# Performance work log

Hardware: AMD Instinct MI355X
Metric: run time of the kernel (lower is better)

The kernel has to match this reference:

```python
import jax, jax.numpy as jnp
import numpy as np

N_HEADS = 12
N_GROUPS = 32
EPS = 1e-5


def setup_inputs() -> dict:
    key = jax.random.key(0)
    ks = jax.random.split(key, 6)
    B, C, H, W = 8, 768, 32, 32
    EC, S = 768, 256
    x = jax.random.normal(ks[0], (B, C, H, W), dtype=jnp.float32)
    encoder_out = jax.random.normal(ks[1], (B, EC, S), dtype=jnp.float32)
    gn_w = jnp.ones((C,), jnp.float32)
    gn_b = jnp.zeros((C,), jnp.float32)
    qkv_w = jax.random.normal(ks[2], (3 * C, C), dtype=jnp.float32) * 0.02
    qkv_b = jnp.zeros((3 * C,), jnp.float32)
    enc_w = jax.random.normal(ks[3], (2 * C, EC), dtype=jnp.float32) * 0.02
    enc_b = jnp.zeros((2 * C,), jnp.float32)
    proj_w = jax.random.normal(ks[4], (C, C), dtype=jnp.float32) * 0.02
    proj_b = jnp.zeros((C,), jnp.float32)
    return {"x": x, "encoder_out": encoder_out, "gn_w": gn_w, "gn_b": gn_b,
            "qkv_w": qkv_w, "qkv_b": qkv_b, "enc_w": enc_w, "enc_b": enc_b,
            "proj_w": proj_w, "proj_b": proj_b}


def _group_norm(x, w, b):
    # x: [B, C, T]
    B, C, T = x.shape
    xg = x.reshape(B, N_GROUPS, C // N_GROUPS, T)
    mean = jnp.mean(xg, axis=(2, 3), keepdims=True)
    var = jnp.var(xg, axis=(2, 3), keepdims=True)
    xn = ((xg - mean) * jax.lax.rsqrt(var + EPS)).reshape(B, C, T)
    return xn * w[None, :, None] + b[None, :, None]


def reference(x, encoder_out, gn_w, gn_b, qkv_w, qkv_b, enc_w, enc_b, proj_w, proj_b):
    B, C, Hs, Ws = x.shape
    T = Hs * Ws
    ch = C // N_HEADS
    xf = x.reshape(B, C, T)
    xn = _group_norm(xf, gn_w, gn_b)
    # 1x1 conv == channel matmul
    qkv = jnp.einsum('oc,bct->bot', qkv_w, xn) + qkv_b[None, :, None]  # [B, 3C, T]
    # torch layout: per-head contiguous blocks of [q, k, v]
    qkv = qkv.reshape(B * N_HEADS, 3 * ch, T)
    q, k, v = qkv[:, :ch], qkv[:, ch:2 * ch], qkv[:, 2 * ch:]
    ekv = jnp.einsum('oc,bcs->bos', enc_w, encoder_out) + enc_b[None, :, None]  # [B, 2C, S]
    ekv = ekv.reshape(B * N_HEADS, 2 * ch, -1)
    ek, ev = ekv[:, :ch], ekv[:, ch:]
    k = jnp.concatenate([ek, k], axis=-1)  # [BH, ch, S+T]
    v = jnp.concatenate([ev, v], axis=-1)
    scale = 1.0 / np.sqrt(np.sqrt(ch))
    w = jnp.einsum('bct,bcs->bts', q * scale, k * scale)  # [BH, T, S+T]
    w = jax.nn.softmax(w.astype(jnp.float32), axis=-1).astype(q.dtype)
    a = jnp.einsum('bts,bcs->bct', w, v).reshape(B, C, T)
    h = jnp.einsum('oc,bct->bot', proj_w, a) + proj_b[None, :, None]
    return (xf + h).reshape(B, C, Hs, Ws)
```

## Files before the change

### kernel.cpp

```cpp
#include <hip/hip_runtime.h>

typedef __attribute__((ext_vector_type(8))) short bf16x8;
typedef __attribute__((ext_vector_type(4))) float f32x4;
typedef __attribute__((ext_vector_type(16))) float f32x16;
typedef __attribute__((ext_vector_type(4))) float float4v;
typedef __attribute__((ext_vector_type(4))) unsigned short ushort4v;
typedef __attribute__((ext_vector_type(8))) unsigned short ushort8v;

#define DEVINL __device__ __forceinline__


DEVINL unsigned short f2bf(float f) {
  union { float f; unsigned u; } v; v.f = f;
  unsigned r = (v.u + 0x7fffu + ((v.u >> 16) & 1u)) >> 16;
  return (unsigned short)r;
}
DEVINL float bf2f(unsigned short h) {
  union { unsigned u; float f; } v; v.u = ((unsigned)h) << 16;
  return v.f;
}
DEVINL float exp2a(float x) {
  float r; asm("v_exp_f32 %0, %1" : "=v"(r) : "v"(x)); return r;
}
DEVINL unsigned cvtpk(float lo, float hi) {
  unsigned r;
  asm("v_cvt_pk_bf16_f32 %0, %1, %2" : "=v"(r) : "v"(lo), "v"(hi));
  return r;
}
DEVINL void gload16(const void* g, void* l) {
  __builtin_amdgcn_global_load_lds(
      (const __attribute__((address_space(1))) unsigned*)g,
      (__attribute__((address_space(3))) unsigned*)l, 16, 0, 0);
}
DEVINL void plswap(unsigned& a, unsigned& b) {
  asm("v_permlane32_swap_b32 %0, %1" : "+v"(a), "+v"(b));
}
DEVINL bf16x8 mkfrag(unsigned a, unsigned b, unsigned c, unsigned d) {
  union { unsigned u[4]; bf16x8 v; } x;
  x.u[0] = a; x.u[1] = b; x.u[2] = c; x.u[3] = d;
  return x.v;
}
#define WAITV0 asm volatile("s_waitcnt vmcnt(0)" ::: "memory")
#define RBAR  __builtin_amdgcn_s_barrier()

__global__ __launch_bounds__(256) void k_cvt3(const float* __restrict__ s0,
                                              const float* __restrict__ s1,
                                              const float* __restrict__ s2,
                                              unsigned short* __restrict__ d) {
  int i = blockIdx.x * 256 + threadIdx.x;
  const float* s; int off;
  if (i < 442368)      { s = s0; off = i; }
  else if (i < 737280) { s = s1; off = i - 442368; }
  else                 { s = s2; off = i - 737280; }
  float4v v = *(const float4v*)(s + (size_t)off * 4);
  ushort4v o;
  o[0] = f2bf(v[0]); o[1] = f2bf(v[1]); o[2] = f2bf(v[2]); o[3] = f2bf(v[3]);
  *(ushort4v*)(d + (size_t)i * 4) = o;
}

__global__ __launch_bounds__(256) void k_gn(const float* __restrict__ x,
                                            const float* __restrict__ gw,
                                            const float* __restrict__ gb,
                                            unsigned short* __restrict__ xnt) {
  int g = blockIdx.x, b = blockIdx.y, tid = threadIdx.x;
  const float* xb = x + ((size_t)b * 768 + g * 24) * 1024;
  float s = 0.f, ss = 0.f;
  for (int i = tid; i < 6144; i += 256) {
    float4v v = *(const float4v*)(xb + (size_t)i * 4);
    s += v[0] + v[1] + v[2] + v[3];
    ss += v[0] * v[0] + v[1] * v[1] + v[2] * v[2] + v[3] * v[3];
  }
  #pragma unroll
  for (int o = 32; o > 0; o >>= 1) { s += __shfl_down(s, o); ss += __shfl_down(ss, o); }
  __shared__ float rs[4], rss[4], stat[2];
  int w = tid >> 6;
  if ((tid & 63) == 0) { rs[w] = s; rss[w] = ss; }
  __syncthreads();
  if (tid == 0) {
    float S = rs[0] + rs[1] + rs[2] + rs[3], SS = rss[0] + rss[1] + rss[2] + rss[3];
    float mean = S / 24576.f;
    float var = SS / 24576.f - mean * mean;
    stat[0] = mean; stat[1] = rsqrtf(fmaxf(var, 0.f) + 1e-5f);
  }
  __syncthreads();
  float mean = stat[0], rstd = stat[1];
  float wv[24], bv[24];
  #pragma unroll
  for (int c = 0; c < 24; ++c) { wv[c] = gw[g * 24 + c]; bv[c] = gb[g * 24 + c]; }
  for (int it = 0; it < 4; ++it) {
    int t = it * 256 + tid;
    ushort8v ov[3];
    #pragma unroll
    for (int c = 0; c < 24; ++c) {
      float v = xb[(size_t)c * 1024 + t];
      ov[c >> 3][c & 7] = f2bf((v - mean) * rstd * wv[c] + bv[c]);
    }
    ushort8v* dst = (ushort8v*)(xnt + ((size_t)(b * 1024 + t)) * 768 + g * 24);
    dst[0] = ov[0]; dst[1] = ov[1]; dst[2] = ov[2];
  }
}

__global__ __launch_bounds__(256) void k_enc_tr(const float* __restrict__ enc,
                                                unsigned short* __restrict__ et) {
  int ct = blockIdx.x * 64, st = blockIdx.y * 64, b = blockIdx.z, tid = threadIdx.x;
  __shared__ unsigned short L[64 * 72];
  #pragma unroll
  for (int it = 0; it < 4; ++it) {
    int idx = it * 256 + tid; int r = idx >> 4, ch = idx & 15;
    float4v v = *(const float4v*)(enc + ((size_t)(b * 768 + ct + r)) * 256 + st + ch * 4);
    ushort4v o;
    o[0] = f2bf(v[0]); o[1] = f2bf(v[1]); o[2] = f2bf(v[2]); o[3] = f2bf(v[3]);
    *(ushort4v*)&L[r * 72 + ch * 4] = o;
  }
  __syncthreads();
  #pragma unroll
  for (int it = 0; it < 2; ++it) {
    int idx = it * 256 + tid; int s = idx >> 3, ch = idx & 7;
    ushort8v o;
    #pragma unroll
    for (int j = 0; j < 8; ++j) o[j] = L[(ch * 8 + j) * 72 + s];
    *(ushort8v*)(et + ((size_t)(b * 256 + st + s)) * 768 + ct + ch * 8) = o;
  }
}

__global__ __launch_bounds__(256) void k_vcat(const unsigned short* __restrict__ qkvt,
                                              const unsigned short* __restrict__ ekvt,
                                              unsigned short* __restrict__ vcat) {
  int s0 = blockIdx.x * 64, bh = blockIdx.y, b = bh / 12, h = bh % 12, tid = threadIdx.x;
  __shared__ unsigned short L[64 * 72];
  #pragma unroll
  for (int it = 0; it < 2; ++it) {
    int idx = it * 256 + tid; int s = idx >> 3, ch = idx & 7;
    int sg = s0 + s;
    const unsigned short* src = (sg < 256)
        ? ekvt + ((size_t)(b * 256 + sg)) * 1536 + h * 128 + 64 + ch * 8
        : qkvt + ((size_t)(b * 1024 + sg - 256)) * 2304 + h * 192 + 128 + ch * 8;
    *(ushort8v*)&L[s * 72 + ch * 8] = *(const ushort8v*)src;
  }
  __syncthreads();
  #pragma unroll
  for (int it = 0; it < 2; ++it) {
    int idx = it * 256 + tid; int c = idx >> 3, ch = idx & 7;
    ushort8v o;
    #pragma unroll
    for (int j = 0; j < 8; ++j) o[j] = L[(ch * 8 + j) * 72 + c];
    *(ushort8v*)(vcat + ((size_t)bh * 64 + c) * 1280 + s0 + ch * 8) = o;
  }
}

template <int EPI, int BM>
__global__ __launch_bounds__(256, 4) void k_gemm(const unsigned short* __restrict__ A,
                                                 const unsigned short* __restrict__ B,
                                                 const float* __restrict__ bias,
                                                 const float* __restrict__ resid,
                                                 void* __restrict__ outp,
                                                 int N, int K,
                                                 long sA, long sB, long sO, long sR) {
  constexpr int MI = BM / 32;
  int bz = blockIdx.z;
  int m0 = blockIdx.x * BM, n0 = blockIdx.y * 128;
  const unsigned short* Ab = A + (size_t)bz * sA + (size_t)m0 * K;
  const unsigned short* Bb = B + (size_t)bz * sB + (size_t)n0 * K;
  __shared__ unsigned short As[2][BM * 32], Bs[2][128 * 32];
  int tid = threadIdx.x, lane = tid & 63, w = tid >> 6;
  int ln = lane & 15, lg = lane >> 4;
  int wm = (w >> 1) * (BM / 2), wn = (w & 1) * 64;
  int sr = tid >> 2, sc = tid & 3;
  const unsigned short* gA = Ab + (size_t)sr * K + ((sc ^ (sr & 3)) * 8);
  const unsigned short* gB = Bb + (size_t)sr * K + ((sc ^ (sr & 3)) * 8);
  int swz = (lg ^ (ln & 3)) * 8;

  f32x4 acc[MI][4];
  #pragma unroll
  for (int i = 0; i < MI; ++i)
    #pragma unroll
    for (int j = 0; j < 4; ++j) acc[i][j] = (f32x4){0.f, 0.f, 0.f, 0.f};

  auto stageAB = [&](int buf, int k0) {
    unsigned short* ad = &As[buf][0] + w * 512;
    unsigned short* bd = &Bs[buf][0] + w * 512;
    gload16(gA + k0, ad);
    if constexpr (BM == 128) gload16(gA + (size_t)64 * K + k0, ad + 2048);
    gload16(gB + k0, bd);
    gload16(gB + (size_t)64 * K + k0, bd + 2048);
  };
  auto WAITP = [&] {
    if constexpr (BM == 128) asm volatile("s_waitcnt vmcnt(4)" ::: "memory");
    else                     asm volatile("s_waitcnt vmcnt(3)" ::: "memory");
  };
  auto comp = [&](int buf) {
    bf16x8 af[MI], bfv[4];
    #pragma unroll
    for (int i = 0; i < MI; ++i) af[i] = *(const bf16x8*)&As[buf][(wm + i * 16 + ln) * 32 + swz];
    #pragma unroll
    for (int j = 0; j < 4; ++j) bfv[j] = *(const bf16x8*)&Bs[buf][(wn + j * 16 + ln) * 32 + swz];
    #pragma unroll
    for (int i = 0; i < MI; ++i)
      #pragma unroll
      for (int j = 0; j < 4; ++j)
        acc[i][j] = __builtin_amdgcn_mfma_f32_16x16x32_bf16(af[i], bfv[j], acc[i][j], 0, 0, 0);
  };

  int nk = K >> 5;
  stageAB(0, 0);
  stageAB(1, 32);
  WAITP();
  RBAR;
  int cur = 0;
  for (int kt = 0; kt < nk; ++kt) {
    comp(cur);
    if (kt + 2 < nk) {
      RBAR;
      stageAB(cur, (kt + 2) * 32);
      WAITP();
      RBAR;
    } else if (kt + 1 < nk) {
      WAITV0;
      RBAR;
    }
    cur ^= 1;
  }

  #pragma unroll
  for (int i = 0; i < MI; ++i) {
    #pragma unroll
    for (int j = 0; j < 4; ++j) {
      #pragma unroll
      for (int r = 0; r < 4; ++r) {
        int row = m0 + wm + i * 16 + lg * 4 + r;
        int col = n0 + wn + j * 16 + ln;
        float v = acc[i][j][r];
        if (EPI == 0) {
          v += bias[col];
          ((unsigned short*)outp)[(size_t)bz * sO + (size_t)row * N + col] = f2bf(v);
        } else {
          v += bias[row] + resid[(size_t)bz * sR + (size_t)row * N + col];
          ((float*)outp)[(size_t)bz * sO + (size_t)row * N + col] = v;
        }
      }
    }
  }
}

__global__ __launch_bounds__(256, 3) void k_attn(const unsigned short* __restrict__ qkvt,
                                                 const unsigned short* __restrict__ ekvt,
                                                 const unsigned short* __restrict__ vcat,
                                                 unsigned short* __restrict__ at) {
  int bid = blockIdx.x;
  int swb = (bid & 7) * 96 + (bid >> 3);
  int t0 = (swb & 7) * 128, bh = swb >> 3, b = bh / 12, h = bh % 12;
  int tid = threadIdx.x, w = tid >> 6, lane = tid & 63;
  int ql = lane & 31, hi = lane >> 5;
  __shared__ unsigned short Ks[2][4096], Vs[2][4096];

  const float QSC = 0.125f * 1.44269504089f;
  bf16x8 aq[4];
  const unsigned short* qrow = qkvt + ((size_t)(b * 1024 + t0 + w * 32 + ql)) * 2304 + h * 192;
  #pragma unroll
  for (int jc = 0; jc < 4; ++jc) {
    ushort8v qv = *(const ushort8v*)(qrow + jc * 16 + hi * 8);
    bf16x8 o;
    #pragma unroll
    for (int e = 0; e < 8; ++e) o[e] = (short)f2bf(bf2f(qv[e]) * QSC);
    aq[jc] = o;
  }

  int rloc = w * 16 + (lane >> 3);
  int chunk = (lane & 7) ^ (lane >> 3);
  const unsigned short* ke_st = ekvt + ((size_t)(b * 256 + rloc)) * 1536 + h * 128 + chunk * 8;
  const unsigned short* kq_st = qkvt + ((long)b * 1024 - 256 + rloc) * 2304 + h * 192 + 64 + chunk * 8;
  const unsigned short* v_st  = vcat + ((size_t)(bh * 64 + rloc)) * 1280 + chunk * 8;
  unsigned short* kd = &Ks[0][0] + w * 1024;
  unsigned short* vd = &Vs[0][0] + w * 1024;

  auto stage = [&](int nb, int tn) {
    const unsigned short* ks;
    size_t rstep;
    if (tn < 4) { ks = ke_st + (size_t)tn * 64 * 1536; rstep = 8 * 1536; }
    else        { ks = kq_st + (size_t)tn * 64 * 2304; rstep = 8 * 2304; }
    unsigned short* kdd = kd + nb * 4096;
    unsigned short* vdd = vd + nb * 4096;
    const unsigned short* vs = v_st + tn * 64;
    gload16(ks, kdd);
    gload16(ks + rstep, kdd + 512);
    gload16(vs, vdd);
    gload16(vs + 8 * 1280, vdd + 512);
  };

  stage(0, 0);
  WAITV0;
  __syncthreads();

  f32x16 acc0, acc1;
  #pragma unroll
  for (int r = 0; r < 16; ++r) { acc0[r] = 0.f; acc1[r] = 0.f; }
  float l = 0.f;
  int xp = (ql & 7) << 4;

  for (int t = 0; t < 20; ++t) {
    int cur = t & 1;
    if (t < 19) stage(cur ^ 1, t + 1);

    f32x16 sA0, sB0, sA1, sB1;
    #pragma unroll
    for (int r = 0; r < 16; ++r) { sA0[r] = 0.f; sB0[r] = 0.f; sA1[r] = 0.f; sB1[r] = 0.f; }
    const char* kbase = (const char*)&Ks[cur][0] + ql * 128;
    __builtin_amdgcn_s_setprio(1);
    #pragma unroll
    for (int jc = 0; jc < 4; ++jc) {
      int off = (jc * 32 + hi * 16) ^ xp;
      bf16x8 k0f = *(const bf16x8*)(kbase + off);
      bf16x8 k1f = *(const bf16x8*)(kbase + 4096 + off);
      if (jc & 1) {
        sB0 = __builtin_amdgcn_mfma_f32_32x32x16_bf16(k0f, aq[jc], sB0, 0, 0, 0);
        sB1 = __builtin_amdgcn_mfma_f32_32x32x16_bf16(k1f, aq[jc], sB1, 0, 0, 0);
      } else {
        sA0 = __builtin_amdgcn_mfma_f32_32x32x16_bf16(k0f, aq[jc], sA0, 0, 0, 0);
        sA1 = __builtin_amdgcn_mfma_f32_32x32x16_bf16(k1f, aq[jc], sA1, 0, 0, 0);
      }
    }
    __builtin_amdgcn_s_setprio(0);
    f32x16 sf0 = sA0 + sB0;
    f32x16 sf1 = sA1 + sB1;

    float pe[32];
    #pragma unroll
    for (int i = 0; i < 16; ++i) pe[i] = exp2a(sf0[i]);
    #pragma unroll
    for (int i = 0; i < 16; ++i) pe[16 + i] = exp2a(sf1[i]);

    const char* vbase = (const char*)&Vs[cur][0] + ql * 128;
    #pragma unroll
    for (int sb = 0; sb < 2; ++sb) {
      unsigned pk[8];
      #pragma unroll
      for (int i = 0; i < 8; ++i)
        pk[i] = cvtpk(pe[sb * 16 + 2 * i], pe[sb * 16 + 2 * i + 1]);
      plswap(pk[0], pk[2]);
      plswap(pk[1], pk[3]);
      plswap(pk[4], pk[6]);
      plswap(pk[5], pk[7]);
      bf16x8 fj0 = mkfrag(pk[0], pk[1], pk[2], pk[3]);
      bf16x8 fj1 = mkfrag(pk[4], pk[5], pk[6], pk[7]);
      __builtin_amdgcn_s_setprio(1);
      #pragma unroll
      for (int jj = 0; jj < 2; ++jj) {
        int off = (sb * 64 + jj * 32 + hi * 16) ^ xp;
        bf16x8 v0f = *(const bf16x8*)(vbase + off);
        bf16x8 v1f = *(const bf16x8*)(vbase + 4096 + off);
        bf16x8 pf = jj ? fj1 : fj0;
        acc0 = __builtin_amdgcn_mfma_f32_32x32x16_bf16(v0f, pf, acc0, 0, 0, 0);
        acc1 = __builtin_amdgcn_mfma_f32_32x32x16_bf16(v1f, pf, acc1, 0, 0, 0);
      }
      __builtin_amdgcn_s_setprio(0);
    }

    float s0 = 0.f, s1 = 0.f, s2 = 0.f, s3 = 0.f;
    #pragma unroll
    for (int i = 0; i < 8; ++i) {
      s0 += pe[i]; s1 += pe[8 + i]; s2 += pe[16 + i]; s3 += pe[24 + i];
    }
    l += (s0 + s1) + (s2 + s3);

    if (t < 19) WAITV0;
    __syncthreads();
  }

  l += __shfl_xor(l, 32);
  float rl = 1.f / l;
  unsigned short* orow = at + ((size_t)(b * 1024 + t0 + w * 32 + ql)) * 768 + h * 64;
  #pragma unroll
  for (int cb = 0; cb < 2; ++cb) {
    #pragma unroll
    for (int g = 0; g < 4; ++g) {
      int c = cb * 32 + g * 8 + hi * 4;
      ushort4v o;
      #pragma unroll
      for (int i = 0; i < 4; ++i) {
        float v = (cb ? acc1[g * 4 + i] : acc0[g * 4 + i]) * rl;
        o[i] = f2bf(v);
      }
      *(ushort4v*)(orow + c) = o;
    }
  }
}

extern "C" void kernel_launch(void* const* d_in, const int* in_sizes, int n_in,
                              void* d_out, int out_size, void* d_ws, size_t ws_size,
                              hipStream_t stream) {
  const float* x      = (const float*)d_in[0];
  const float* enc    = (const float*)d_in[1];
  const float* gn_w   = (const float*)d_in[2];
  const float* gn_b   = (const float*)d_in[3];
  const float* qkv_w  = (const float*)d_in[4];
  const float* qkv_b  = (const float*)d_in[5];
  const float* enc_w  = (const float*)d_in[6];
  const float* enc_b  = (const float*)d_in[7];
  const float* proj_w = (const float*)d_in[8];
  const float* proj_b = (const float*)d_in[9];
  float* out = (float*)d_out;

  char* ws = (char*)d_ws;
  unsigned short* w_qkv = (unsigned short*)(ws + 0);
  unsigned short* w_enc = (unsigned short*)(ws + 3538944);
  unsigned short* w_prj = (unsigned short*)(ws + 5898240);
  unsigned short* xn_t  = (unsigned short*)(ws + 7077888);
  unsigned short* enc_t = (unsigned short*)(ws + 19660800);
  unsigned short* qkv_t = (unsigned short*)(ws + 22806528);
  unsigned short* ekv_t = (unsigned short*)(ws + 60555264);
  unsigned short* vcat  = (unsigned short*)(ws + 66846720);
  unsigned short* a_t   = xn_t;

  k_cvt3<<<3456, 256, 0, stream>>>(qkv_w, enc_w, proj_w, w_qkv);
  k_gn<<<dim3(32, 8), 256, 0, stream>>>(x, gn_w, gn_b, xn_t);
  k_enc_tr<<<dim3(12, 4, 8), 256, 0, stream>>>(enc, enc_t);
  k_gemm<0, 128><<<dim3(64, 18, 1), 256, 0, stream>>>(xn_t, w_qkv, qkv_b, nullptr, qkv_t,
                                                      2304, 768, 0L, 0L, 0L, 0L);
  k_gemm<0, 64><<<dim3(32, 12, 1), 256, 0, stream>>>(enc_t, w_enc, enc_b, nullptr, ekv_t,
                                                     1536, 768, 0L, 0L, 0L, 0L);
  k_vcat<<<dim3(20, 96), 256, 0, stream>>>(qkv_t, ekv_t, vcat);
  k_attn<<<dim3(768), 256, 0, stream>>>(qkv_t, ekv_t, vcat, a_t);
  k_gemm<1, 64><<<dim3(12, 8, 8), 256, 0, stream>>>(w_prj, a_t, proj_b, x, out,
                                                    1024, 768, 0L, 786432L, 786432L, 786432L);
}
```

Before: 174.3 us.

## Software-pipeline attention: triple-buffer K/V and overlap next QK with current PV

Moves the attention loop to a three-stage LDS ring buffer. It prefetches two tiles ahead and computes the next tile's QK scores before the current tile's exp/PV work, so MFMA and exp/pack work from different tiles can interleave. The exp-sum is folded into the pack loop and the split A/B accumulators for QK are dropped. This costs more LDS (which may reduce occupancy at 3 blocks/CU), more live registers for the carried score tiles, and a serial MFMA dependency chain in QK.

```diff
diff --git a/kernel.cpp b/kernel.cpp
--- a/kernel.cpp
+++ b/kernel.cpp
@@ -41,6 +41,7 @@
   return x.v;
 }
 #define WAITV0 asm volatile("s_waitcnt vmcnt(0)" ::: "memory")
+#define WAITV4 asm volatile("s_waitcnt vmcnt(4)" ::: "memory")
 #define RBAR  __builtin_amdgcn_s_barrier()
 
 __global__ __launch_bounds__(256) void k_cvt3(const float* __restrict__ s0,
@@ -251,7 +252,7 @@
   int t0 = (swb & 7) * 128, bh = swb >> 3, b = bh / 12, h = bh % 12;
   int tid = threadIdx.x, w = tid >> 6, lane = tid & 63;
   int ql = lane & 31, hi = lane >> 5;
-  __shared__ unsigned short Ks[2][4096], Vs[2][4096];
+  __shared__ unsigned short Ks[3][4096], Vs[3][4096];
 
   const float QSC = 0.125f * 1.44269504089f;
   bf16x8 aq[4];
@@ -270,16 +271,14 @@
   const unsigned short* ke_st = ekvt + ((size_t)(b * 256 + rloc)) * 1536 + h * 128 + chunk * 8;
   const unsigned short* kq_st = qkvt + ((long)b * 1024 - 256 + rloc) * 2304 + h * 192 + 64 + chunk * 8;
   const unsigned short* v_st  = vcat + ((size_t)(bh * 64 + rloc)) * 1280 + chunk * 8;
-  unsigned short* kd = &Ks[0][0] + w * 1024;
-  unsigned short* vd = &Vs[0][0] + w * 1024;
 
   auto stage = [&](int nb, int tn) {
     const unsigned short* ks;
     size_t rstep;
     if (tn < 4) { ks = ke_st + (size_t)tn * 64 * 1536; rstep = 8 * 1536; }
     else        { ks = kq_st + (size_t)tn * 64 * 2304; rstep = 8 * 2304; }
-    unsigned short* kdd = kd + nb * 4096;
-    unsigned short* vdd = vd + nb * 4096;
+    unsigned short* kdd = &Ks[nb][0] + w * 1024;
+    unsigned short* vdd = &Vs[nb][0] + w * 1024;
     const unsigned short* vs = v_st + tn * 64;
     gload16(ks, kdd);
     gload16(ks + rstep, kdd + 512);
@@ -287,55 +286,54 @@
     gload16(vs + 8 * 1280, vdd + 512);
   };
 
-  stage(0, 0);
-  WAITV0;
-  __syncthreads();
-
-  f32x16 acc0, acc1;
-  #pragma unroll
-  for (int r = 0; r < 16; ++r) { acc0[r] = 0.f; acc1[r] = 0.f; }
-  float l = 0.f;
   int xp = (ql & 7) << 4;
-
-  for (int t = 0; t < 20; ++t) {
-    int cur = t & 1;
-    if (t < 19) stage(cur ^ 1, t + 1);
-
-    f32x16 sA0, sB0, sA1, sB1;
-    #pragma unroll
-    for (int r = 0; r < 16; ++r) { sA0[r] = 0.f; sB0[r] = 0.f; sA1[r] = 0.f; sB1[r] = 0.f; }
-    const char* kbase = (const char*)&Ks[cur][0] + ql * 128;
+  auto qk = [&](int nb, f32x16& s0v, f32x16& s1v) {
+    const char* kbase = (const char*)&Ks[nb][0] + ql * 128;
     __builtin_amdgcn_s_setprio(1);
     #pragma unroll
     for (int jc = 0; jc < 4; ++jc) {
       int off = (jc * 32 + hi * 16) ^ xp;
       bf16x8 k0f = *(const bf16x8*)(kbase + off);
       bf16x8 k1f = *(const bf16x8*)(kbase + 4096 + off);
-      if (jc & 1) {
-        sB0 = __builtin_amdgcn_mfma_f32_32x32x16_bf16(k0f, aq[jc], sB0, 0, 0, 0);
-        sB1 = __builtin_amdgcn_mfma_f32_32x32x16_bf16(k1f, aq[jc], sB1, 0, 0, 0);
-      } else {
-        sA0 = __builtin_amdgcn_mfma_f32_32x32x16_bf16(k0f, aq[jc], sA0, 0, 0, 0);
-        sA1 = __builtin_amdgcn_mfma_f32_32x32x16_bf16(k1f, aq[jc], sA1, 0, 0, 0);
-      }
+      s0v = __builtin_amdgcn_mfma_f32_32x32x16_bf16(k0f, aq[jc], s0v, 0, 0, 0);
+      s1v = __builtin_amdgcn_mfma_f32_32x32x16_bf16(k1f, aq[jc], s1v, 0, 0, 0);
     }
     __builtin_amdgcn_s_setprio(0);
-    f32x16 sf0 = sA0 + sB0;
-    f32x16 sf1 = sA1 + sB1;
-
-    float pe[32];
-    #pragma unroll
-    for (int i = 0; i < 16; ++i) pe[i] = exp2a(sf0[i]);
-    #pragma unroll
-    for (int i = 0; i < 16; ++i) pe[16 + i] = exp2a(sf1[i]);
-
-    const char* vbase = (const char*)&Vs[cur][0] + ql * 128;
+  };
+
+  f32x16 acc0, acc1, sfP0, sfP1;
+  #pragma unroll
+  for (int r = 0; r < 16; ++r) { acc0[r] = 0.f; acc1[r] = 0.f; sfP0[r] = 0.f; sfP1[r] = 0.f; }
+  float l = 0.f;
+
+  stage(0, 0);
+  stage(1, 1);
+  WAITV4;
+  __syncthreads();
+  qk(0, sfP0, sfP1);
+
+  for (int t = 0; t < 20; ++t) {
+    if (t < 19) WAITV0;
+    __syncthreads();
+
+    f32x16 sN0, sN1;
+    #pragma unroll
+    for (int r = 0; r < 16; ++r) { sN0[r] = 0.f; sN1[r] = 0.f; }
+    if (t < 19) qk((t + 1) % 3, sN0, sN1);
+
+    if (t + 2 < 20) stage((t + 2) % 3, t + 2);
+
+    const char* vbase = (const char*)&Vs[t % 3][0] + ql * 128;
     #pragma unroll
     for (int sb = 0; sb < 2; ++sb) {
       unsigned pk[8];
       #pragma unroll
-      for (int i = 0; i < 8; ++i)
-        pk[i] = cvtpk(pe[sb * 16 + 2 * i], pe[sb * 16 + 2 * i + 1]);
+      for (int i = 0; i < 8; ++i) {
+        float ea = exp2a(sb ? sfP1[2 * i] : sfP0[2 * i]);
+        float eb = exp2a(sb ? sfP1[2 * i + 1] : sfP0[2 * i + 1]);
+        l += ea + eb;
+        pk[i] = cvtpk(ea, eb);
+      }
       plswap(pk[0], pk[2]);
       plswap(pk[1], pk[3]);
       plswap(pk[4], pk[6]);
@@ -355,15 +353,8 @@
       __builtin_amdgcn_s_setprio(0);
     }
 
-    float s0 = 0.f, s1 = 0.f, s2 = 0.f, s3 = 0.f;
-    #pragma unroll
-    for (int i = 0; i < 8; ++i) {
-      s0 += pe[i]; s1 += pe[8 + i]; s2 += pe[16 + i]; s3 += pe[24 + i];
-    }
-    l += (s0 + s1) + (s2 + s3);
-
-    if (t < 19) WAITV0;
-    __syncthreads();
+    sfP0 = sN0;
+    sfP1 = sN1;
   }
 
   l += __shfl_xor(l, 32);
```

New measurement: 177.4 us. About the same (+1.8%).

## Switch GEMM to 32x32 MFMA with triple-buffered LDS pipeline; simplify attention accumulators

Applied to the files above, without the earlier changes.

The projection GEMM kernel now uses 32x32x16 MFMA tiles instead of 16x16x32, with a new LDS swizzle and a matching epilogue index mapping. The K loop moves from double to triple buffering, so the next tile is staged before compute and each iteration needs only one barrier. Occupancy drops from 4 to 3 blocks per CU because of the larger LDS footprint. The attention QK^T loop now uses a single accumulator chain per tile instead of two split chains followed by an add, which removes vector adds but serializes the MFMA dependencies.

```diff
diff --git a/kernel.cpp b/kernel.cpp
--- a/kernel.cpp
+++ b/kernel.cpp
@@ -149,32 +149,34 @@
 }
 
 template <int EPI, int BM>
-__global__ __launch_bounds__(256, 4) void k_gemm(const unsigned short* __restrict__ A,
+__global__ __launch_bounds__(256, 3) void k_gemm(const unsigned short* __restrict__ A,
                                                  const unsigned short* __restrict__ B,
                                                  const float* __restrict__ bias,
                                                  const float* __restrict__ resid,
                                                  void* __restrict__ outp,
                                                  int N, int K,
                                                  long sA, long sB, long sO, long sR) {
-  constexpr int MI = BM / 32;
+  constexpr int R32 = BM / 64;
   int bz = blockIdx.z;
   int m0 = blockIdx.x * BM, n0 = blockIdx.y * 128;
   const unsigned short* Ab = A + (size_t)bz * sA + (size_t)m0 * K;
   const unsigned short* Bb = B + (size_t)bz * sB + (size_t)n0 * K;
-  __shared__ unsigned short As[2][BM * 32], Bs[2][128 * 32];
+  __shared__ unsigned short As[3][BM * 32], Bs[3][128 * 32];
   int tid = threadIdx.x, lane = tid & 63, w = tid >> 6;
-  int ln = lane & 15, lg = lane >> 4;
+  int l31 = lane & 31, hi2 = lane >> 5;
   int wm = (w >> 1) * (BM / 2), wn = (w & 1) * 64;
   int sr = tid >> 2, sc = tid & 3;
-  const unsigned short* gA = Ab + (size_t)sr * K + ((sc ^ (sr & 3)) * 8);
-  const unsigned short* gB = Bb + (size_t)sr * K + ((sc ^ (sr & 3)) * 8);
-  int swz = (lg ^ (ln & 3)) * 8;
-
-  f32x4 acc[MI][4];
-  #pragma unroll
-  for (int i = 0; i < MI; ++i)
-    #pragma unroll
-    for (int j = 0; j < 4; ++j) acc[i][j] = (f32x4){0.f, 0.f, 0.f, 0.f};
+  int schunk = (sc ^ ((sr >> 1) & 3)) * 8;
+  const unsigned short* gA = Ab + (size_t)sr * K + schunk;
+  const unsigned short* gB = Bb + (size_t)sr * K + schunk;
+
+  f32x16 acc[R32][2];
+  #pragma unroll
+  for (int i = 0; i < R32; ++i)
+    #pragma unroll
+    for (int j = 0; j < 2; ++j)
+      #pragma unroll
+      for (int r = 0; r < 16; ++r) acc[i][j][r] = 0.f;
 
   auto stageAB = [&](int buf, int k0) {
     unsigned short* ad = &As[buf][0] + w * 512;
@@ -189,16 +191,30 @@
     else                     asm volatile("s_waitcnt vmcnt(3)" ::: "memory");
   };
   auto comp = [&](int buf) {
-    bf16x8 af[MI], bfv[4];
-    #pragma unroll
-    for (int i = 0; i < MI; ++i) af[i] = *(const bf16x8*)&As[buf][(wm + i * 16 + ln) * 32 + swz];
-    #pragma unroll
-    for (int j = 0; j < 4; ++j) bfv[j] = *(const bf16x8*)&Bs[buf][(wn + j * 16 + ln) * 32 + swz];
-    #pragma unroll
-    for (int i = 0; i < MI; ++i)
-      #pragma unroll
-      for (int j = 0; j < 4; ++j)
-        acc[i][j] = __builtin_amdgcn_mfma_f32_16x16x32_bf16(af[i], bfv[j], acc[i][j], 0, 0, 0);
+    const char* abase = (const char*)&As[buf][0];
+    const char* bbase = (const char*)&Bs[buf][0];
+    #pragma unroll
+    for (int kk = 0; kk < 2; ++kk) {
+      bf16x8 afr[R32], bfr[2];
+      #pragma unroll
+      for (int ri = 0; ri < R32; ++ri) {
+        int row = wm + ri * 32 + l31;
+        int sl = (kk * 2 + hi2) ^ ((row >> 1) & 3);
+        afr[ri] = *(const bf16x8*)(abase + row * 64 + sl * 16);
+      }
+      #pragma unroll
+      for (int ci = 0; ci < 2; ++ci) {
+        int row = wn + ci * 32 + l31;
+        int sl = (kk * 2 + hi2) ^ ((row >> 1) & 3);
+        bfr[ci] = *(const bf16x8*)(bbase + row * 64 + sl * 16);
+      }
+      #pragma unroll
+      for (int ri = 0; ri < R32; ++ri)
+        #pragma unroll
+        for (int ci = 0; ci < 2; ++ci)
+          acc[ri][ci] = __builtin_amdgcn_mfma_f32_32x32x16_bf16(afr[ri], bfr[ci],
+                                                                acc[ri][ci], 0, 0, 0);
+    }
   };
 
   int nk = K >> 5;
@@ -207,29 +223,29 @@
   WAITP();
   RBAR;
   int cur = 0;
-  for (int kt = 0; kt < nk; ++kt) {
+  for (int kt = 0; kt < nk - 2; ++kt) {
+    int pre = cur - 1; if (pre < 0) pre += 3;
+    stageAB(pre, (kt + 2) * 32);
     comp(cur);
-    if (kt + 2 < nk) {
-      RBAR;
-      stageAB(cur, (kt + 2) * 32);
-      WAITP();
-      RBAR;
-    } else if (kt + 1 < nk) {
-      WAITV0;
-      RBAR;
-    }
-    cur ^= 1;
-  }
-
-  #pragma unroll
-  for (int i = 0; i < MI; ++i) {
-    #pragma unroll
-    for (int j = 0; j < 4; ++j) {
-      #pragma unroll
-      for (int r = 0; r < 4; ++r) {
-        int row = m0 + wm + i * 16 + lg * 4 + r;
-        int col = n0 + wn + j * 16 + ln;
-        float v = acc[i][j][r];
+    WAITP();
+    RBAR;
+    ++cur; if (cur == 3) cur = 0;
+  }
+  comp(cur);
+  WAITV0;
+  RBAR;
+  ++cur; if (cur == 3) cur = 0;
+  comp(cur);
+
+  #pragma unroll
+  for (int ri = 0; ri < R32; ++ri) {
+    #pragma unroll
+    for (int ci = 0; ci < 2; ++ci) {
+      #pragma unroll
+      for (int rg = 0; rg < 16; ++rg) {
+        int row = m0 + wm + ri * 32 + (rg & 3) + 8 * (rg >> 2) + 4 * hi2;
+        int col = n0 + wn + ci * 32 + l31;
+        float v = acc[ri][ci][rg];
         if (EPI == 0) {
           v += bias[col];
           ((unsigned short*)outp)[(size_t)bz * sO + (size_t)row * N + col] = f2bf(v);
@@ -301,9 +317,9 @@
     int cur = t & 1;
     if (t < 19) stage(cur ^ 1, t + 1);
 
-    f32x16 sA0, sB0, sA1, sB1;
-    #pragma unroll
-    for (int r = 0; r < 16; ++r) { sA0[r] = 0.f; sB0[r] = 0.f; sA1[r] = 0.f; sB1[r] = 0.f; }
+    f32x16 sf0, sf1;
+    #pragma unroll
+    for (int r = 0; r < 16; ++r) { sf0[r] = 0.f; sf1[r] = 0.f; }
     const char* kbase = (const char*)&Ks[cur][0] + ql * 128;
     __builtin_amdgcn_s_setprio(1);
     #pragma unroll
@@ -311,17 +327,10 @@
       int off = (jc * 32 + hi * 16) ^ xp;
       bf16x8 k0f = *(const bf16x8*)(kbase + off);
       bf16x8 k1f = *(const bf16x8*)(kbase + 4096 + off);
-      if (jc & 1) {
-        sB0 = __builtin_amdgcn_mfma_f32_32x32x16_bf16(k0f, aq[jc], sB0, 0, 0, 0);
-        sB1 = __builtin_amdgcn_mfma_f32_32x32x16_bf16(k1f, aq[jc], sB1, 0, 0, 0);
-      } else {
-        sA0 = __builtin_amdgcn_mfma_f32_32x32x16_bf16(k0f, aq[jc], sA0, 0, 0, 0);
-        sA1 = __builtin_amdgcn_mfma_f32_32x32x16_bf16(k1f, aq[jc], sA1, 0, 0, 0);
-      }
+      sf0 = __builtin_amdgcn_mfma_f32_32x32x16_bf16(k0f, aq[jc], sf0, 0, 0, 0);
+      sf1 = __builtin_amdgcn_mfma_f32_32x32x16_bf16(k1f, aq[jc], sf1, 0, 0, 0);
     }
     __builtin_amdgcn_s_setprio(0);
-    f32x16 sf0 = sA0 + sB0;
-    f32x16 sf1 = sA1 + sB1;
 
     float pe[32];
     #pragma unroll
```

After: 168.1 us. 3.6% less time.
